# Kernel tuning notes

Measured on AMD Instinct MI355X. Metric: run time of the kernel, lower is better.

The kernel has to match this reference:

```python
import jax, jax.numpy as jnp
import numpy as np

H = 64      # h_dim
E = 64      # embedding_dim
L = 100     # latent_dim
T = 30      # seq_len
DT = 0.03

def _leaky(x):
    return jnp.where(x >= 0, x, 0.01 * x)  # nn.LeakyReLU default slope

def _mlp(h, Ws, bs, Wf, bf):
    # 3 stacked [H,H] LeakyReLU layers + final [L,H] layer, LeakyReLU after EVERY layer (as in source)
    for i in range(Ws.shape[0]):
        h = _leaky(h @ Ws[i].T + bs[i])
    return _leaky(h @ Wf.T + bf)

def _lstm_step(h, c, gates):
    # torch LSTM gate order: i, f, g, o
    i, f, g, o = jnp.split(gates, 4, axis=-1)
    c = jax.nn.sigmoid(f) * c + jax.nn.sigmoid(i) * jnp.tanh(g)
    h = jax.nn.sigmoid(o) * jnp.tanh(c)
    return h, c

def _forward(expert_traj, init_state, eps,
             W_se, b_se,
             W_ih_e, W_hh_e, b_ih_e, b_hh_e,
             mean_Ws, mean_bs, mean_Wf, mean_bf,
             lv_Ws, lv_bs, lv_Wf, lv_bf,
             W_init, b_init,
             W_ih_d, W_hh_d, b_ih_d, b_hh_d,
             W_c, b_c):
    B = expert_traj.shape[0]
    # --- encode: relative positions ---
    rel_xy = jnp.concatenate([expert_traj[:, :1, :2],
                              expert_traj[:, 1:, :2] - expert_traj[:, :-1, :2]], axis=1)
    inp = jnp.concatenate([rel_xy, expert_traj[:, :, 2:]], axis=-1)  # [B,T,4]
    emb = inp @ W_se.T + b_se                                        # [B,T,E]
    x_seq = jnp.swapaxes(emb, 0, 1)                                  # [T,B,E] seq-major
    # precompute input projection for all timesteps in one GEMM
    xp = x_seq @ W_ih_e.T + (b_ih_e + b_hh_e)                        # [T,B,4H]
    h0 = jnp.zeros((B, H), dtype=expert_traj.dtype)
    c0 = jnp.zeros((B, H), dtype=expert_traj.dtype)
    def enc_step(carry, xp_t):
        h, c = carry
        h, c = _lstm_step(h, c, xp_t + h @ W_hh_e.T)
        return (h, c), None
    (hT, _), _ = jax.lax.scan(enc_step, (h0, c0), xp)
    mu = _mlp(hT, mean_Ws, mean_bs, mean_Wf, mean_bf)                # [B,L]
    log_var = _mlp(hT, lv_Ws, lv_bs, lv_Wf, lv_bf)                   # [B,L]
    # --- reparameterize + tanh ---
    z = jnp.tanh(eps * jnp.exp(0.5 * log_var) + mu)
    # --- decode ---
    dh = z @ W_init.T + b_init                                       # [B,H], h0 = c0 = dh
    bias_d = b_ih_d + b_hh_d
    def dec_step(carry, _):
        h, c, prev = carry
        xe = prev @ W_se.T + b_se                                    # spatial embedding of state
        h, c = _lstm_step(h, c, xe @ W_ih_d.T + h @ W_hh_d.T + bias_d)
        ctrl = h @ W_c.T + b_c                                       # [B,2]
        pedal = ctrl[:, 0]
        steer = jnp.clip(ctrl[:, 1], -0.5, 0.5)
        x_t, y_t, psi, v = prev[:, 0], prev[:, 1], prev[:, 2], prev[:, 3]
        v1 = jnp.clip(v + pedal * DT, 0.0, 30.0)
        psi_dot = jnp.clip(v * jnp.tan(steer) / 2.5, -3.14 / 2, 3.14 / 2)
        cur = jnp.stack([x_t + v * jnp.cos(psi) * DT,
                         y_t + v * jnp.sin(psi) * DT,
                         psi + psi_dot * DT,
                         v1], axis=1)
        return (h, c, cur), cur
    _, traj = jax.lax.scan(dec_step, (dh, dh, init_state), None, length=T)
    recons = jnp.swapaxes(traj, 0, 1)                                # [B,T,4]
    return recons, expert_traj, mu, log_var

def setup_inputs() -> dict:
    key = jax.random.key(0)
    ks = jax.random.split(key, 32)
    B = 16384
    s = 0.05
    def p(k, shape):
        return jax.random.normal(k, shape, dtype=jnp.float32) * s
    return {
        "expert_traj": jax.random.normal(ks[0], (B, T, 4), dtype=jnp.float32),
        "init_state": jax.random.normal(ks[1], (B, 4), dtype=jnp.float32),
        "eps": jax.random.normal(ks[2], (B, L), dtype=jnp.float32),
        "W_se": p(ks[3], (E, 4)), "b_se": p(ks[4], (E,)),
        "W_ih_e": p(ks[5], (4 * H, E)), "W_hh_e": p(ks[6], (4 * H, H)),
        "b_ih_e": p(ks[7], (4 * H,)), "b_hh_e": p(ks[8], (4 * H,)),
        "mean_Ws": p(ks[9], (3, H, H)), "mean_bs": p(ks[10], (3, H)),
        "mean_Wf": p(ks[11], (L, H)), "mean_bf": p(ks[12], (L,)),
        "lv_Ws": p(ks[13], (3, H, H)), "lv_bs": p(ks[14], (3, H)),
        "lv_Wf": p(ks[15], (L, H)), "lv_bf": p(ks[16], (L,)),
        "W_init": p(ks[17], (H, L)), "b_init": p(ks[18], (H,)),
        "W_ih_d": p(ks[19], (4 * H, E)), "W_hh_d": p(ks[20], (4 * H, H)),
        "b_ih_d": p(ks[21], (4 * H,)), "b_hh_d": p(ks[22], (4 * H,)),
        "W_c": p(ks[23], (2, H)), "b_c": p(ks[24], (2,)),
    }

def reference(expert_traj, init_state, eps,
              W_se, b_se,
              W_ih_e, W_hh_e, b_ih_e, b_hh_e,
              mean_Ws, mean_bs, mean_Wf, mean_bf,
              lv_Ws, lv_bs, lv_Wf, lv_bf,
              W_init, b_init,
              W_ih_d, W_hh_d, b_ih_d, b_hh_d,
              W_c, b_c):
    return _forward(expert_traj, init_state, eps,
                    W_se, b_se,
                    W_ih_e, W_hh_e, b_ih_e, b_hh_e,
                    mean_Ws, mean_bs, mean_Wf, mean_bf,
                    lv_Ws, lv_bs, lv_Wf, lv_bf,
                    W_init, b_init,
                    W_ih_d, W_hh_d, b_ih_d, b_hh_d,
                    W_c, b_c)
```

## Files before the change

### kernel.cpp

```cpp
#include <hip/hip_runtime.h>

typedef unsigned short u16;
typedef unsigned int u32;
typedef __attribute__((ext_vector_type(8))) short bf16x8;
typedef __attribute__((ext_vector_type(4))) float f32x4;

#define B_TOT 16384
#define RR 32
#define NBLK (B_TOT / RR)
#define TT 30
#define LL 100
#define DTC 0.03f
#define L2E 1.44269504088896f

#define HST 104
#define HBUF_U16 (RR * HST)

#define OFF_H   0
#define OFF_XB  13312
#define OFF_Z   22528
#define OFF_U   31232
#define SMEM_SZ 38912

#define WS_WHHE  0
#define WS_WHHD  18432
#define WS_MWS   36864
#define WS_LWS   49152
#define WS_MWF   61440
#define WS_LWF   67840
#define WS_WINIT 74240
#define WS_TOTAL 82432

__device__ __forceinline__ float bf2f(u16 u) {
    union { u32 i; float f; } v; v.i = ((u32)u) << 16; return v.f;
}
__device__ __forceinline__ u16 f2bf(float f) {
    union { float f; u32 i; } v; v.f = f;
    return (u16)((v.i + 0x7FFFu + ((v.i >> 16) & 1u)) >> 16);
}
__device__ __forceinline__ u16 f2bf_t(float f) {
    union { float f; u32 i; } v; v.f = f;
    return (u16)(v.i >> 16);
}
__device__ __forceinline__ float rcpf(float x) { return __builtin_amdgcn_rcpf(x); }
__device__ __forceinline__ float ex2(float x) { return __builtin_amdgcn_exp2f(x); }
__device__ __forceinline__ float tanh_(float x) {
    x = fminf(fmaxf(x, -15.f), 15.f);
    float e = __expf(2.f * x);
    return (e - 1.f) * rcpf(e + 1.f);
}
__device__ __forceinline__ float leaky(float x) { return x >= 0.f ? x : 0.01f * x; }
__device__ __forceinline__ f32x4 mfma16(bf16x8 a, bf16x8 b, f32x4 c) {
    return __builtin_amdgcn_mfma_f32_16x16x32_bf16(a, b, c, 0, 0, 0);
}

__global__ void setup_kernel(
    const float* __restrict__ W_se, const float* __restrict__ b_se,
    const float* __restrict__ W_ih_e, const float* __restrict__ W_hh_e,
    const float* __restrict__ b_ih_e, const float* __restrict__ b_hh_e,
    const float* __restrict__ W_ih_d, const float* __restrict__ W_hh_d,
    const float* __restrict__ b_ih_d, const float* __restrict__ b_hh_d,
    const float* __restrict__ mean_Ws, const float* __restrict__ lv_Ws,
    const float* __restrict__ mean_Wf, const float* __restrict__ lv_Wf,
    const float* __restrict__ W_init, u16* __restrict__ ws)
{
    const int gid = blockIdx.x * 256 + threadIdx.x;
    const int nth = gridDim.x * 256;
    for (int i = gid; i < 512; i += nth) {
        int which = i >> 8, row = i & 255, g = row >> 6;
        float s = (g == 2) ? 2.f * L2E : L2E;
        const float* wih = (which ? W_ih_d : W_ih_e) + row * 64;
        float f0=0,f1=0,f2=0,f3=0,fb=0;
        for (int e = 0; e < 64; ++e) {
            float w = wih[e];
            f0 = fmaf(w, W_se[e*4+0], f0);
            f1 = fmaf(w, W_se[e*4+1], f1);
            f2 = fmaf(w, W_se[e*4+2], f2);
            f3 = fmaf(w, W_se[e*4+3], f3);
            fb = fmaf(w, b_se[e], fb);
        }
        fb += (which ? b_ih_d : b_ih_e)[row] + (which ? b_hh_d : b_hh_e)[row];
        u16* dst = ws + (which ? WS_WHHD : WS_WHHE) + row * 72 + 64;
        dst[0]=f2bf(f0*s); dst[1]=f2bf(f1*s); dst[2]=f2bf(f2*s); dst[3]=f2bf(f3*s);
        dst[4]=f2bf(fb*s); dst[5]=0; dst[6]=0; dst[7]=0;
    }
    for (int i = gid; i < 2*16384; i += nth) {
        int which = i >= 16384;
        int j = which ? i - 16384 : i;
        int row = j >> 6, k = j & 63, g = row >> 6;
        float s = (g == 2) ? 2.f * L2E : L2E;
        const float* whh = which ? W_hh_d : W_hh_e;
        ws[(which ? WS_WHHD : WS_WHHE) + row*72 + k] = f2bf(whh[j] * s);
    }
    for (int i = gid; i < 12288; i += nth) {
        ws[WS_MWS + i] = f2bf(mean_Ws[i]);
        ws[WS_LWS + i] = f2bf(lv_Ws[i]);
    }
    for (int i = gid; i < 6400; i += nth) {
        ws[WS_MWF + i] = f2bf(mean_Wf[i]);
        ws[WS_LWF + i] = f2bf(lv_Wf[i]);
    }
    for (int i = gid; i < 8192; i += nth) {
        int r = i >> 7, k = i & 127;
        ws[WS_WINIT + i] = (k < LL) ? f2bf(W_init[r*LL + k]) : (u16)0;
    }
}

__global__ __launch_bounds__(256, 2) void vae_lstm_kernel(
    const float* __restrict__ expert, const float* __restrict__ init_state,
    const float* __restrict__ eps, const u16* __restrict__ ws,
    const float* __restrict__ mean_bs, const float* __restrict__ mean_bf,
    const float* __restrict__ lv_bs, const float* __restrict__ lv_bf,
    const float* __restrict__ b_init, const float* __restrict__ W_c,
    const float* __restrict__ b_c,
    float* __restrict__ out_recons, float* __restrict__ out_expert,
    float* __restrict__ out_mu, float* __restrict__ out_lv)
{
    const int tid = threadIdx.x;
    const int b0g = blockIdx.x * RR;
    const int wv = tid >> 6;
    const int lane = tid & 63;
    const int lcol = lane & 15;
    const int quad = lane >> 4;
    const int jcol = wv * 16 + lcol;

    __shared__ __align__(16) char smem[SMEM_SZ];
    u16* Hbuf  = (u16*)(smem + OFF_H);
    u16* XB0   = (u16*)(smem + OFF_XB);
    u16* XB1   = XB0 + RR * 72;
    u16* zBuf  = (u16*)(smem + OFF_Z);
    u16* inp   = (u16*)(smem + OFF_U);
    u16* muB   = (u16*)(smem + OFF_U);
    float* sRaw  = (float*)(smem + OFF_XB);
    float* sPrev = (float*)(smem + OFF_XB);
    float* sWc   = (float*)(smem + OFF_XB + 512);

    {
        const int base = b0g * (TT*4);
        u32* hz = (u32*)Hbuf;
        for (int idx = tid; idx < HBUF_U16; idx += 256) hz[idx] = 0;
        for (int idx = tid; idx < RR*TT*4; idx += 256) {
            float v = expert[base + idx];
            sRaw[idx] = v;
            out_expert[base + idx] = v;
        }
        __syncthreads();
        for (int idx = tid; idx < RR*TT*4; idx += 256) {
            int q = idx % (TT*4);
            int k = q & 3, t = q >> 2;
            int row = idx / (TT*4);
            float v = sRaw[idx];
            if (k < 2 && t > 0) v -= sRaw[idx - 4];
            u16 hv = f2bf(v);
            inp[idx] = hv;
            if (t == 0) Hbuf[row*HST + 64 + k] = hv;
            if (q == 0) {
                Hbuf[row*HST + 68] = 0x3F80;
                Hbuf[HBUF_U16 + row*HST + 68] = 0x3F80;
            }
        }
        __syncthreads();
    }

    float creg[8];
#pragma unroll
    for (int u = 0; u < 8; ++u) creg[u] = 0.f;
    bf16x8 bw[4][3];

    auto build_bw = [&](const u16* wsW) {
#pragma unroll
        for (int g = 0; g < 4; ++g) {
            const u16* wr = wsW + (g*64 + jcol) * 72;
            bw[g][0] = *(const bf16x8*)(wr + quad*8);
            bw[g][1] = *(const bf16x8*)(wr + 32 + quad*8);
            if (quad == 0) {
                bw[g][2] = *(const bf16x8*)(wr + 64);
            } else {
                bf16x8 z;
#pragma unroll
                for (int j = 0; j < 8; ++j) z[j] = 0;
                bw[g][2] = z;
            }
        }
    };

    auto lstm_step = [&](const u16* Hc, u16* Hn) {
        f32x4 acc[2][4];
#pragma unroll
        for (int c = 0; c < 2; ++c) {
            bf16x8 a0 = *(const bf16x8*)(Hc + (c*16 + lcol)*HST + quad*8);
            bf16x8 a1 = *(const bf16x8*)(Hc + (c*16 + lcol)*HST + 32 + quad*8);
            bf16x8 a2 = *(const bf16x8*)(Hc + (c*16 + lcol)*HST + 64 + quad*8);
#pragma unroll
            for (int g = 0; g < 4; ++g) {
                f32x4 z = {0.f, 0.f, 0.f, 0.f};
                z = mfma16(a0, bw[g][0], z);
                z = mfma16(a1, bw[g][1], z);
                acc[c][g] = mfma16(a2, bw[g][2], z);
            }
        }
#pragma unroll
        for (int c = 0; c < 2; ++c)
#pragma unroll
            for (int r = 0; r < 4; ++r) {
                float Ei = ex2(-acc[c][0][r]);
                float Ef = ex2(-acc[c][1][r]);
                float Eg = ex2(-acc[c][2][r]);
                float Eo = ex2(-acc[c][3][r]);
                float P = (1.f + Ei) * (1.f + Eg);
                float Q = 1.f + Ef;
                float num = fmaf(creg[c*4 + r], P, (1.f - Eg) * Q);
                float cc = num * rcpf(P * Q);
                creg[c*4 + r] = cc;
                float Ec = ex2(-2.f * L2E * cc);
                float h = (1.f - Ec) * rcpf((1.f + Eo) * (1.f + Ec));
                Hn[(c*16 + quad*4 + r)*HST + jcol] = f2bf_t(h);
            }
    };

    build_bw(ws + WS_WHHE);
    for (int stp = 0; stp < TT; ++stp) {
        const u16* Hc = Hbuf + (stp & 1) * HBUF_U16;
        u16* Hn = Hbuf + ((stp + 1) & 1) * HBUF_U16;
        lstm_step(Hc, Hn);
        if (tid < 128 && stp < TT-1) {
            int row = tid >> 2, k = tid & 3;
            Hn[row*HST + 64 + k] = inp[row*(TT*4) + (stp+1)*4 + k];
        }
        __syncthreads();
    }

    {
        u32* zb = (u32*)zBuf;
        for (int idx = tid; idx < RR*136/2; idx += 256) zb[idx] = 0;
    }

    auto mlp_hidden = [&](const u16* inB, int inStride, u16* outB,
                          const u16* wsW, const float* bg) {
        float bv = bg[jcol];
        const u16* wr = wsW + jcol*64;
        bf16x8 bb0 = *(const bf16x8*)(wr + quad*8);
        bf16x8 bb1 = *(const bf16x8*)(wr + 32 + quad*8);
#pragma unroll
        for (int Mt = 0; Mt < 2; ++Mt) {
            f32x4 acc = {bv, bv, bv, bv};
            bf16x8 a0 = *(const bf16x8*)(inB + (Mt*16 + lcol)*inStride + quad*8);
            bf16x8 a1 = *(const bf16x8*)(inB + (Mt*16 + lcol)*inStride + 32 + quad*8);
            acc = mfma16(a0, bb0, acc);
            acc = mfma16(a1, bb1, acc);
#pragma unroll
            for (int r = 0; r < 4; ++r)
                outB[(Mt*16 + quad*4 + r)*72 + jcol] = f2bf_t(leaky(acc[r]));
        }
        __syncthreads();
    };

    auto mlp_final = [&](const u16* inB, const u16* wsW, const float* bg, int mode) {
#pragma unroll
        for (int ni = 0; ni < 2; ++ni) {
            int nt = wv + ni*4;
            if (nt >= 7) continue;
            int n = nt*16 + lcol;
            bool ok = (n < LL);
            float bv = ok ? bg[n] : 0.f;
            bf16x8 bb0, bb1;
            if (ok) {
                const u16* wr = wsW + n*64;
                bb0 = *(const bf16x8*)(wr + quad*8);
                bb1 = *(const bf16x8*)(wr + 32 + quad*8);
            } else {
#pragma unroll
                for (int j = 0; j < 8; ++j) { bb0[j] = 0; bb1[j] = 0; }
            }
#pragma unroll
            for (int Mt = 0; Mt < 2; ++Mt) {
                f32x4 acc = {bv, bv, bv, bv};
                bf16x8 a0 = *(const bf16x8*)(inB + (Mt*16 + lcol)*72 + quad*8);
                bf16x8 a1 = *(const bf16x8*)(inB + (Mt*16 + lcol)*72 + 32 + quad*8);
                acc = mfma16(a0, bb0, acc);
                acc = mfma16(a1, bb1, acc);
                if (ok) {
#pragma unroll
                    for (int r = 0; r < 4; ++r) {
                        int m = Mt*16 + quad*4 + r;
                        float vv = leaky(acc[r]);
                        size_t gi = (size_t)(b0g + m) * LL + n;
                        if (mode == 0) {
                            muB[m*LL + n] = f2bf_t(vv);
                            out_mu[gi] = vv;
                        } else {
                            out_lv[gi] = vv;
                            float mu = bf2f(muB[m*LL + n]);
                            float zv = tanh_(fmaf(eps[gi], __expf(0.5f * vv), mu));
                            zBuf[m*136 + n] = f2bf_t(zv);
                        }
                    }
                }
            }
        }
        __syncthreads();
    };

    mlp_hidden(Hbuf, HST, XB0, ws + WS_MWS, mean_bs);
    mlp_hidden(XB0, 72, XB1, ws + WS_MWS + 4096, mean_bs + 64);
    mlp_hidden(XB1, 72, XB0, ws + WS_MWS + 8192, mean_bs + 128);
    mlp_final(XB0, ws + WS_MWF, mean_bf, 0);
    mlp_hidden(Hbuf, HST, XB0, ws + WS_LWS, lv_bs);
    mlp_hidden(XB0, 72, XB1, ws + WS_LWS + 4096, lv_bs + 64);
    mlp_hidden(XB1, 72, XB0, ws + WS_LWS + 8192, lv_bs + 128);
    mlp_final(XB0, ws + WS_LWF, lv_bf, 1);

    {
        float bv = b_init[jcol];
        const u16* wr = ws + WS_WINIT + jcol*128;
#pragma unroll
        for (int Mt = 0; Mt < 2; ++Mt) {
            f32x4 acc = {bv, bv, bv, bv};
#pragma unroll
            for (int kt = 0; kt < 4; ++kt) {
                bf16x8 az = *(const bf16x8*)(zBuf + (Mt*16 + lcol)*136 + kt*32 + quad*8);
                bf16x8 bi = *(const bf16x8*)(wr + kt*32 + quad*8);
                acc = mfma16(az, bi, acc);
            }
#pragma unroll
            for (int r = 0; r < 4; ++r) {
                creg[Mt*4 + r] = acc[r];
                Hbuf[(Mt*16 + quad*4 + r)*HST + jcol] = f2bf_t(acc[r]);
            }
        }
        __syncthreads();
        if (tid < RR*4) {
            float v = init_state[b0g*4 + tid];
            sPrev[tid] = v;
            Hbuf[(tid >> 2)*HST + 64 + (tid & 3)] = f2bf(v);
        }
        if (tid < 128) sWc[tid] = W_c[tid];
        __syncthreads();
    }

    build_bw(ws + WS_WHHD);
    const float bc0 = b_c[0], bc1 = b_c[1];

    for (int stp = 0; stp < TT; ++stp) {
        const u16* Hc = Hbuf + (stp & 1) * HBUF_U16;
        u16* Hn = Hbuf + ((stp + 1) & 1) * HBUF_U16;
        lstm_step(Hc, Hn);
        __syncthreads();
        if (tid < 128) {
            int row = tid >> 2, kq = tid & 3;
            const u16* hr = Hn + row*HST + kq*16;
            bf16x8 h0 = *(const bf16x8*)(hr);
            bf16x8 h1 = *(const bf16x8*)(hr + 8);
            const float4* w0 = (const float4*)(sWc + kq*16);
            const float4* w1 = (const float4*)(sWc + 64 + kq*16);
            float a0 = 0.f, a1 = 0.f;
#pragma unroll
            for (int p = 0; p < 2; ++p) {
                float4 wa = w0[2*p], wb = w0[2*p+1];
                float4 va = w1[2*p], vb = w1[2*p+1];
                bf16x8 hh = p ? h1 : h0;
                float hf[8];
#pragma unroll
                for (int j = 0; j < 8; ++j) hf[j] = bf2f((u16)hh[j]);
                a0 = fmaf(hf[0], wa.x, a0); a0 = fmaf(hf[1], wa.y, a0);
                a0 = fmaf(hf[2], wa.z, a0); a0 = fmaf(hf[3], wa.w, a0);
                a0 = fmaf(hf[4], wb.x, a0); a0 = fmaf(hf[5], wb.y, a0);
                a0 = fmaf(hf[6], wb.z, a0); a0 = fmaf(hf[7], wb.w, a0);
                a1 = fmaf(hf[0], va.x, a1); a1 = fmaf(hf[1], va.y, a1);
                a1 = fmaf(hf[2], va.z, a1); a1 = fmaf(hf[3], va.w, a1);
                a1 = fmaf(hf[4], vb.x, a1); a1 = fmaf(hf[5], vb.y, a1);
                a1 = fmaf(hf[6], vb.z, a1); a1 = fmaf(hf[7], vb.w, a1);
            }
            a0 += __shfl_xor(a0, 1); a1 += __shfl_xor(a1, 1);
            a0 += __shfl_xor(a0, 2); a1 += __shfl_xor(a1, 2);
            if (kq == 0) {
                float pedal = a0 + bc0;
                float steer = fminf(fmaxf(a1 + bc1, -0.5f), 0.5f);
                float4 pv = *(const float4*)(sPrev + row*4);
                float x = pv.x, y = pv.y, psi = pv.z, v = pv.w;
                float v1 = fminf(fmaxf(v + pedal * DTC, 0.f), 30.f);
                float sn, cs;
                __sincosf(psi, &sn, &cs);
                float psid = fminf(fmaxf(v * __tanf(steer) * 0.4f, -1.57f), 1.57f);
                float nx = fmaf(v * cs, DTC, x);
                float ny = fmaf(v * sn, DTC, y);
                float npsi = fmaf(psid, DTC, psi);
                float4 o; o.x = nx; o.y = ny; o.z = npsi; o.w = v1;
                *(float4*)(sPrev + row*4) = o;
                *(float4*)(out_recons + ((size_t)(b0g + row) * TT + stp) * 4) = o;
                u32 lo = (u32)f2bf(nx) | ((u32)f2bf(ny) << 16);
                u32 hi = (u32)f2bf(npsi) | ((u32)f2bf(v1) << 16);
                uint2 pk; pk.x = lo; pk.y = hi;
                *(uint2*)(Hn + row*HST + 64) = pk;
            }
        }
        __syncthreads();
    }
}

extern "C" void kernel_launch(void* const* d_in, const int* in_sizes, int n_in,
                              void* d_out, int out_size, void* d_ws, size_t ws_size,
                              hipStream_t stream) {
    (void)in_sizes; (void)n_in; (void)ws_size; (void)out_size;
    const float* expert    = (const float*)d_in[0];
    const float* init_st   = (const float*)d_in[1];
    const float* eps       = (const float*)d_in[2];
    const float* W_se      = (const float*)d_in[3];
    const float* b_se      = (const float*)d_in[4];
    const float* W_ih_e    = (const float*)d_in[5];
    const float* W_hh_e    = (const float*)d_in[6];
    const float* b_ih_e    = (const float*)d_in[7];
    const float* b_hh_e    = (const float*)d_in[8];
    const float* mean_Ws   = (const float*)d_in[9];
    const float* mean_bs   = (const float*)d_in[10];
    const float* mean_Wf   = (const float*)d_in[11];
    const float* mean_bf   = (const float*)d_in[12];
    const float* lv_Ws     = (const float*)d_in[13];
    const float* lv_bs     = (const float*)d_in[14];
    const float* lv_Wf     = (const float*)d_in[15];
    const float* lv_bf     = (const float*)d_in[16];
    const float* W_init    = (const float*)d_in[17];
    const float* b_init    = (const float*)d_in[18];
    const float* W_ih_d    = (const float*)d_in[19];
    const float* W_hh_d    = (const float*)d_in[20];
    const float* b_ih_d    = (const float*)d_in[21];
    const float* b_hh_d    = (const float*)d_in[22];
    const float* W_c       = (const float*)d_in[23];
    const float* b_c       = (const float*)d_in[24];

    float* out = (float*)d_out;
    const size_t n_traj = (size_t)B_TOT * TT * 4;
    const size_t n_lat  = (size_t)B_TOT * LL;
    float* out_recons = out;
    float* out_expert = out + n_traj;
    float* out_mu     = out + 2 * n_traj;
    float* out_lv     = out + 2 * n_traj + n_lat;

    u16* ws = (u16*)d_ws;

    setup_kernel<<<64, 256, 0, stream>>>(
        W_se, b_se, W_ih_e, W_hh_e, b_ih_e, b_hh_e,
        W_ih_d, W_hh_d, b_ih_d, b_hh_d,
        mean_Ws, lv_Ws, mean_Wf, lv_Wf, W_init, ws);

    vae_lstm_kernel<<<NBLK, 256, 0, stream>>>(
        expert, init_st, eps, ws,
        mean_bs, mean_bf, lv_bs, lv_bf, b_init, W_c, b_c,
        out_recons, out_expert, out_mu, out_lv);
}
```

Before: 219.2 us.

## Split each block's row tiles across twice as many waves (512 threads)

After: 209.7 us. -4.3%, faster.

```diff
diff --git a/kernel.cpp b/kernel.cpp
--- a/kernel.cpp
+++ b/kernel.cpp
@@ -7,6 +7,7 @@
 
 #define B_TOT 16384
 #define RR 32
+#define BLK 512
 #define NBLK (B_TOT / RR)
 #define TT 30
 #define LL 100
@@ -106,7 +107,7 @@
     }
 }
 
-__global__ __launch_bounds__(256, 2) void vae_lstm_kernel(
+__global__ __launch_bounds__(BLK, 4) void vae_lstm_kernel(
     const float* __restrict__ expert, const float* __restrict__ init_state,
     const float* __restrict__ eps, const u16* __restrict__ ws,
     const float* __restrict__ mean_bs, const float* __restrict__ mean_bf,
@@ -119,10 +120,12 @@
     const int tid = threadIdx.x;
     const int b0g = blockIdx.x * RR;
     const int wv = tid >> 6;
+    const int Mt = wv >> 2;
+    const int wsub = wv & 3;
     const int lane = tid & 63;
     const int lcol = lane & 15;
     const int quad = lane >> 4;
-    const int jcol = wv * 16 + lcol;
+    const int jcol = wsub * 16 + lcol;
 
     __shared__ __align__(16) char smem[SMEM_SZ];
     u16* Hbuf  = (u16*)(smem + OFF_H);
@@ -138,14 +141,14 @@
     {
         const int base = b0g * (TT*4);
         u32* hz = (u32*)Hbuf;
-        for (int idx = tid; idx < HBUF_U16; idx += 256) hz[idx] = 0;
-        for (int idx = tid; idx < RR*TT*4; idx += 256) {
+        for (int idx = tid; idx < HBUF_U16; idx += BLK) hz[idx] = 0;
+        for (int idx = tid; idx < RR*TT*4; idx += BLK) {
             float v = expert[base + idx];
             sRaw[idx] = v;
             out_expert[base + idx] = v;
         }
         __syncthreads();
-        for (int idx = tid; idx < RR*TT*4; idx += 256) {
+        for (int idx = tid; idx < RR*TT*4; idx += BLK) {
             int q = idx % (TT*4);
             int k = q & 3, t = q >> 2;
             int row = idx / (TT*4);
@@ -162,9 +165,7 @@
         __syncthreads();
     }
 
-    float creg[8];
-#pragma unroll
-    for (int u = 0; u < 8; ++u) creg[u] = 0.f;
+    float creg[4] = {0.f, 0.f, 0.f, 0.f};
     bf16x8 bw[4][3];
 
     auto build_bw = [&](const u16* wsW) {
@@ -185,37 +186,33 @@
     };
 
     auto lstm_step = [&](const u16* Hc, u16* Hn) {
-        f32x4 acc[2][4];
-#pragma unroll
-        for (int c = 0; c < 2; ++c) {
-            bf16x8 a0 = *(const bf16x8*)(Hc + (c*16 + lcol)*HST + quad*8);
-            bf16x8 a1 = *(const bf16x8*)(Hc + (c*16 + lcol)*HST + 32 + quad*8);
-            bf16x8 a2 = *(const bf16x8*)(Hc + (c*16 + lcol)*HST + 64 + quad*8);
-#pragma unroll
-            for (int g = 0; g < 4; ++g) {
-                f32x4 z = {0.f, 0.f, 0.f, 0.f};
-                z = mfma16(a0, bw[g][0], z);
-                z = mfma16(a1, bw[g][1], z);
-                acc[c][g] = mfma16(a2, bw[g][2], z);
-            }
-        }
-#pragma unroll
-        for (int c = 0; c < 2; ++c)
-#pragma unroll
-            for (int r = 0; r < 4; ++r) {
-                float Ei = ex2(-acc[c][0][r]);
-                float Ef = ex2(-acc[c][1][r]);
-                float Eg = ex2(-acc[c][2][r]);
-                float Eo = ex2(-acc[c][3][r]);
-                float P = (1.f + Ei) * (1.f + Eg);
-                float Q = 1.f + Ef;
-                float num = fmaf(creg[c*4 + r], P, (1.f - Eg) * Q);
-                float cc = num * rcpf(P * Q);
-                creg[c*4 + r] = cc;
-                float Ec = ex2(-2.f * L2E * cc);
-                float h = (1.f - Ec) * rcpf((1.f + Eo) * (1.f + Ec));
-                Hn[(c*16 + quad*4 + r)*HST + jcol] = f2bf_t(h);
-            }
+        const u16* hrow = Hc + (Mt*16 + lcol)*HST;
+        bf16x8 a0 = *(const bf16x8*)(hrow + quad*8);
+        bf16x8 a1 = *(const bf16x8*)(hrow + 32 + quad*8);
+        bf16x8 a2 = *(const bf16x8*)(hrow + 64 + quad*8);
+        f32x4 acc[4];
+#pragma unroll
+        for (int g = 0; g < 4; ++g) {
+            f32x4 z = {0.f, 0.f, 0.f, 0.f};
+            z = mfma16(a0, bw[g][0], z);
+            z = mfma16(a1, bw[g][1], z);
+            acc[g] = mfma16(a2, bw[g][2], z);
+        }
+#pragma unroll
+        for (int r = 0; r < 4; ++r) {
+            float Ei = ex2(-acc[0][r]);
+            float Ef = ex2(-acc[1][r]);
+            float Eg = ex2(-acc[2][r]);
+            float Eo = ex2(-acc[3][r]);
+            float P = (1.f + Ei) * (1.f + Eg);
+            float Q = 1.f + Ef;
+            float num = fmaf(creg[r], P, (1.f - Eg) * Q);
+            float cc = num * rcpf(P * Q);
+            creg[r] = cc;
+            float Ec = ex2(-2.f * L2E * cc);
+            float h = (1.f - Ec) * rcpf((1.f + Eo) * (1.f + Ec));
+            Hn[(Mt*16 + quad*4 + r)*HST + jcol] = f2bf_t(h);
+        }
     };
 
     build_bw(ws + WS_WHHE);
@@ -232,7 +229,7 @@
 
     {
         u32* zb = (u32*)zBuf;
-        for (int idx = tid; idx < RR*136/2; idx += 256) zb[idx] = 0;
+        for (int idx = tid; idx < RR*136/2; idx += BLK) zb[idx] = 0;
     }
 
     auto mlp_hidden = [&](const u16* inB, int inStride, u16* outB,
@@ -241,25 +238,23 @@
         const u16* wr = wsW + jcol*64;
         bf16x8 bb0 = *(const bf16x8*)(wr + quad*8);
         bf16x8 bb1 = *(const bf16x8*)(wr + 32 + quad*8);
-#pragma unroll
-        for (int Mt = 0; Mt < 2; ++Mt) {
-            f32x4 acc = {bv, bv, bv, bv};
-            bf16x8 a0 = *(const bf16x8*)(inB + (Mt*16 + lcol)*inStride + quad*8);
-            bf16x8 a1 = *(const bf16x8*)(inB + (Mt*16 + lcol)*inStride + 32 + quad*8);
-            acc = mfma16(a0, bb0, acc);
-            acc = mfma16(a1, bb1, acc);
-#pragma unroll
-            for (int r = 0; r < 4; ++r)
-                outB[(Mt*16 + quad*4 + r)*72 + jcol] = f2bf_t(leaky(acc[r]));
-        }
+        f32x4 acc = {bv, bv, bv, bv};
+        bf16x8 a0 = *(const bf16x8*)(inB + (Mt*16 + lcol)*inStride + quad*8);
+        bf16x8 a1 = *(const bf16x8*)(inB + (Mt*16 + lcol)*inStride + 32 + quad*8);
+        acc = mfma16(a0, bb0, acc);
+        acc = mfma16(a1, bb1, acc);
+#pragma unroll
+        for (int r = 0; r < 4; ++r)
+            outB[(Mt*16 + quad*4 + r)*72 + jcol] = f2bf_t(leaky(acc[r]));
         __syncthreads();
     };
 
     auto mlp_final = [&](const u16* inB, const u16* wsW, const float* bg, int mode) {
 #pragma unroll
-        for (int ni = 0; ni < 2; ++ni) {
-            int nt = wv + ni*4;
-            if (nt >= 7) continue;
+        for (int ti = 0; ti < 2; ++ti) {
+            int t = wv + ti*8;
+            if (t >= 14) continue;
+            int nt = t >> 1, Mtl = t & 1;
             int n = nt*16 + lcol;
             bool ok = (n < LL);
             float bv = ok ? bg[n] : 0.f;
@@ -272,28 +267,25 @@
 #pragma unroll
                 for (int j = 0; j < 8; ++j) { bb0[j] = 0; bb1[j] = 0; }
             }
-#pragma unroll
-            for (int Mt = 0; Mt < 2; ++Mt) {
-                f32x4 acc = {bv, bv, bv, bv};
-                bf16x8 a0 = *(const bf16x8*)(inB + (Mt*16 + lcol)*72 + quad*8);
-                bf16x8 a1 = *(const bf16x8*)(inB + (Mt*16 + lcol)*72 + 32 + quad*8);
-                acc = mfma16(a0, bb0, acc);
-                acc = mfma16(a1, bb1, acc);
-                if (ok) {
-#pragma unroll
-                    for (int r = 0; r < 4; ++r) {
-                        int m = Mt*16 + quad*4 + r;
-                        float vv = leaky(acc[r]);
-                        size_t gi = (size_t)(b0g + m) * LL + n;
-                        if (mode == 0) {
-                            muB[m*LL + n] = f2bf_t(vv);
-                            out_mu[gi] = vv;
-                        } else {
-                            out_lv[gi] = vv;
-                            float mu = bf2f(muB[m*LL + n]);
-                            float zv = tanh_(fmaf(eps[gi], __expf(0.5f * vv), mu));
-                            zBuf[m*136 + n] = f2bf_t(zv);
-                        }
+            f32x4 acc = {bv, bv, bv, bv};
+            bf16x8 a0 = *(const bf16x8*)(inB + (Mtl*16 + lcol)*72 + quad*8);
+            bf16x8 a1 = *(const bf16x8*)(inB + (Mtl*16 + lcol)*72 + 32 + quad*8);
+            acc = mfma16(a0, bb0, acc);
+            acc = mfma16(a1, bb1, acc);
+            if (ok) {
+#pragma unroll
+                for (int r = 0; r < 4; ++r) {
+                    int m = Mtl*16 + quad*4 + r;
+                    float vv = leaky(acc[r]);
+                    size_t gi = (size_t)(b0g + m) * LL + n;
+                    if (mode == 0) {
+                        muB[m*LL + n] = f2bf_t(vv);
+                        out_mu[gi] = vv;
+                    } else {
+                        out_lv[gi] = vv;
+                        float mu = bf2f(muB[m*LL + n]);
+                        float zv = tanh_(fmaf(eps[gi], __expf(0.5f * vv), mu));
+                        zBuf[m*136 + n] = f2bf_t(zv);
                     }
                 }
             }
@@ -313,20 +305,17 @@
     {
         float bv = b_init[jcol];
         const u16* wr = ws + WS_WINIT + jcol*128;
-#pragma unroll
-        for (int Mt = 0; Mt < 2; ++Mt) {
-            f32x4 acc = {bv, bv, bv, bv};
-#pragma unroll
-            for (int kt = 0; kt < 4; ++kt) {
-                bf16x8 az = *(const bf16x8*)(zBuf + (Mt*16 + lcol)*136 + kt*32 + quad*8);
-                bf16x8 bi = *(const bf16x8*)(wr + kt*32 + quad*8);
-                acc = mfma16(az, bi, acc);
-            }
-#pragma unroll
-            for (int r = 0; r < 4; ++r) {
-                creg[Mt*4 + r] = acc[r];
-                Hbuf[(Mt*16 + quad*4 + r)*HST + jcol] = f2bf_t(acc[r]);
-            }
+        f32x4 acc = {bv, bv, bv, bv};
+#pragma unroll
+        for (int kt = 0; kt < 4; ++kt) {
+            bf16x8 az = *(const bf16x8*)(zBuf + (Mt*16 + lcol)*136 + kt*32 + quad*8);
+            bf16x8 bi = *(const bf16x8*)(wr + kt*32 + quad*8);
+            acc = mfma16(az, bi, acc);
+        }
+#pragma unroll
+        for (int r = 0; r < 4; ++r) {
+            creg[r] = acc[r];
+            Hbuf[(Mt*16 + quad*4 + r)*HST + jcol] = f2bf_t(acc[r]);
         }
         __syncthreads();
         if (tid < RR*4) {
@@ -443,7 +432,7 @@
         W_ih_d, W_hh_d, b_ih_d, b_hh_d,
         mean_Ws, lv_Ws, mean_Wf, lv_Wf, W_init, ws);
 
-    vae_lstm_kernel<<<NBLK, 256, 0, stream>>>(
+    vae_lstm_kernel<<<NBLK, BLK, 0, stream>>>(
         expert, init_st, eps, ws,
         mean_bs, mean_bf, lv_bs, lv_bf, b_init, W_c, b_c,
         out_recons, out_expert, out_mu, out_lv);
```
